# Optimization experiments

Measured on AMD Instinct MI355X. Metric: run time of the kernel, lower is better.

Reference implementation:

```python
import jax, jax.numpy as jnp
import numpy as np

LN_EPS = 1e-5

def _layernorm(w, g, b):
    mu = jnp.mean(w, axis=-1, keepdims=True)
    var = jnp.mean(jnp.square(w - mu), axis=-1, keepdims=True)
    return (w - mu) * jax.lax.rsqrt(var + LN_EPS) * g + b

def _ligru_layer(x, W, U, g, b):
    # x: [B, T, F]; W: [2H, F]; U: [2H, H]
    B = x.shape[0]
    H = U.shape[1]
    w = jnp.einsum('btf,hf->bth', x, W)          # [B, T, 2H]
    w = _layernorm(w, g, b)
    h0 = jnp.zeros((B, H), dtype=x.dtype)

    def step(h, w_t):                            # w_t: [B, 2H]
        gates = w_t + h @ U.T
        at, zt = gates[:, :H], gates[:, H:]
        zt = jax.nn.sigmoid(zt)
        hcand = jax.nn.relu(at)
        h = zt * h + (1.0 - zt) * hcand
        return h, h

    _, hs = jax.lax.scan(step, h0, jnp.swapaxes(w, 0, 1))  # hs: [T, B, H]
    return jnp.swapaxes(hs, 0, 1)                # [B, T, H]

def setup_inputs() -> dict:
    key = jax.random.key(0)
    ks = jax.random.split(key, 5)
    B, T, F, H = 16, 1500, 80, 512
    x = jax.random.normal(ks[0], (B, T, F), dtype=jnp.float32)
    W0 = jax.random.normal(ks[1], (2 * H, F), dtype=jnp.float32) / np.sqrt(F)
    U0 = jax.random.normal(ks[2], (2 * H, H), dtype=jnp.float32) / np.sqrt(H)
    W1 = jax.random.normal(ks[3], (2 * H, H), dtype=jnp.float32) / np.sqrt(H)
    U1 = jax.random.normal(ks[4], (2 * H, H), dtype=jnp.float32) / np.sqrt(H)
    g0 = jnp.ones((2 * H,), jnp.float32); b0 = jnp.zeros((2 * H,), jnp.float32)
    g1 = jnp.ones((2 * H,), jnp.float32); b1 = jnp.zeros((2 * H,), jnp.float32)
    return {"x": x, "W0": W0, "U0": U0, "g0": g0, "b0": b0,
            "W1": W1, "U1": U1, "g1": g1, "b1": b1}

def reference(x, W0, U0, g0, b0, W1, U1, g1, b1):
    h = _ligru_layer(x, W0, U0, g0, b0)
    h = _ligru_layer(h, W1, U1, g1, b1)
    return h
```

## Files before the change

kernel.cpp:

```cpp
#include <hip/hip_runtime.h>
#include <cstddef>
#include <cstdint>

#define kB 16
#define kT 1500
#define kF 80
#define kH 512
#define kGG 1024
#define kM (kB * kT)

__global__ __launch_bounds__(256) void gemm_nt_k(
    const float* __restrict__ A, const float* __restrict__ Bt,
    float* __restrict__ C, int K) {
  __shared__ float As[16][68];
  __shared__ float Bs[16][68];
  const int tid = threadIdx.x;
  const int m0 = blockIdx.x * 64;
  const int n0 = blockIdx.y * 64;
  const int tx = tid & 15;
  const int ty = tid >> 4;
  const int r  = tid >> 2;
  const int q  = tid & 3;
  float acc[4][4] = {};
  for (int k0 = 0; k0 < K; k0 += 16) {
    const float4 va = *(const float4*)&A [(size_t)(m0 + r) * K + k0 + q * 4];
    const float4 vb = *(const float4*)&Bt[(size_t)(n0 + r) * K + k0 + q * 4];
    __syncthreads();
    As[q * 4 + 0][r] = va.x; As[q * 4 + 1][r] = va.y;
    As[q * 4 + 2][r] = va.z; As[q * 4 + 3][r] = va.w;
    Bs[q * 4 + 0][r] = vb.x; Bs[q * 4 + 1][r] = vb.y;
    Bs[q * 4 + 2][r] = vb.z; Bs[q * 4 + 3][r] = vb.w;
    __syncthreads();
#pragma unroll
    for (int kk = 0; kk < 16; ++kk) {
      const float4 a = *(const float4*)&As[kk][ty * 4];
      const float4 b = *(const float4*)&Bs[kk][tx * 4];
      acc[0][0] += a.x * b.x; acc[0][1] += a.x * b.y; acc[0][2] += a.x * b.z; acc[0][3] += a.x * b.w;
      acc[1][0] += a.y * b.x; acc[1][1] += a.y * b.y; acc[1][2] += a.y * b.z; acc[1][3] += a.y * b.w;
      acc[2][0] += a.z * b.x; acc[2][1] += a.z * b.y; acc[2][2] += a.z * b.z; acc[2][3] += a.z * b.w;
      acc[3][0] += a.w * b.x; acc[3][1] += a.w * b.y; acc[3][2] += a.w * b.z; acc[3][3] += a.w * b.w;
    }
  }
#pragma unroll
  for (int i = 0; i < 4; ++i) {
    float4 o;
    o.x = acc[i][0]; o.y = acc[i][1]; o.z = acc[i][2]; o.w = acc[i][3];
    *(float4*)&C[(size_t)(m0 + ty * 4 + i) * kGG + n0 + tx * 4] = o;
  }
}

__global__ __launch_bounds__(256) void ln_rows(
    float* __restrict__ w, const float* __restrict__ g,
    const float* __restrict__ bb) {
  const int row = blockIdx.x;
  float4* p = (float4*)(w + (size_t)row * kGG);
  const int tid = threadIdx.x;
  float4 v = p[tid];
  float s  = v.x + v.y + v.z + v.w;
  float s2 = v.x * v.x + v.y * v.y + v.z * v.z + v.w * v.w;
#pragma unroll
  for (int off = 32; off >= 1; off >>= 1) {
    s  += __shfl_down(s, off);
    s2 += __shfl_down(s2, off);
  }
  __shared__ float red[8];
  const int lane = tid & 63, wv = tid >> 6;
  if (lane == 0) { red[wv] = s; red[4 + wv] = s2; }
  __syncthreads();
  s  = red[0] + red[1] + red[2] + red[3];
  s2 = red[4] + red[5] + red[6] + red[7];
  const float mu  = s * (1.f / kGG);
  const float var = s2 * (1.f / kGG) - mu * mu;
  const float rs  = rsqrtf(var + 1e-5f);
  const float4 gg = ((const float4*)g)[tid];
  const float4 bv = ((const float4*)bb)[tid];
  v.x = (v.x - mu) * rs * gg.x + bv.x;
  v.y = (v.y - mu) * rs * gg.y + bv.y;
  v.z = (v.z - mu) * rs * gg.z + bv.z;
  v.w = (v.w - mu) * rs * gg.w + bv.w;
  p[tid] = v;
}

__global__ __launch_bounds__(256, 1) void ligru_scan(
    const float* __restrict__ wn,
    const float* __restrict__ U,
    float* __restrict__ hist) {
  const int blk  = blockIdx.x;
  const int b    = blk >> 4;
  const int jblk = blk & 15;
  const int tid  = threadIdx.x;
  const int ks   = tid & 7;
  const int jj   = tid >> 3;
  const int j    = jblk * 32 + jj;
  const int k0   = ks * 64;

  __shared__ float hsh[2][8 * 68];

  float4 ua[16], uz[16];
#pragma unroll
  for (int q = 0; q < 16; ++q) {
    ua[q] = *(const float4*)&U[(size_t)j * kH + k0 + q * 4];
    uz[q] = *(const float4*)&U[(size_t)(j + kH) * kH + k0 + q * 4];
  }

  const float* wrow = wn + (size_t)b * kT * kGG;
  float* hrow = hist + (size_t)b * kT * kH;

  const int w0 = 2 * tid;
  const int lc = (w0 >> 6) * 68 + (w0 & 63);

  float hprev = 0.f;

  for (int t = 0; t < kT; ++t) {
    float wa = 0.f, wz = 0.f;
    if (ks == 0) {
      wa = wrow[(size_t)t * kGG + j];
      wz = wrow[(size_t)t * kGG + kH + j];
    }

    float* dst = hsh[t & 1];
    if (t == 0) {
      *(float2*)&dst[lc] = make_float2(0.f, 0.f);
    } else {
      const int* hp = (const int*)(hrow + (size_t)(t - 1) * kH);
      int v0, v1;
      do {
        v0 = __hip_atomic_load(hp + w0,     __ATOMIC_RELAXED,
                               __HIP_MEMORY_SCOPE_AGENT);
        v1 = __hip_atomic_load(hp + w0 + 1, __ATOMIC_RELAXED,
                               __HIP_MEMORY_SCOPE_AGENT);
      } while ((v0 | v1) < 0);
      *(float2*)&dst[lc] = make_float2(__int_as_float(v0), __int_as_float(v1));
    }
    __syncthreads();

    const float* src = dst + ks * 68;
    float ga = 0.f, gz = 0.f;
#pragma unroll
    for (int q = 0; q < 16; ++q) {
      const float4 h4 = *(const float4*)&src[q * 4];
      ga += h4.x * ua[q].x + h4.y * ua[q].y + h4.z * ua[q].z + h4.w * ua[q].w;
      gz += h4.x * uz[q].x + h4.y * uz[q].y + h4.z * uz[q].z + h4.w * uz[q].w;
    }
#pragma unroll
    for (int off = 1; off < 8; off <<= 1) {
      ga += __shfl_xor(ga, off);
      gz += __shfl_xor(gz, off);
    }

    if (ks == 0) {
      const float a    = wa + ga;
      const float z    = wz + gz;
      const float zt   = 1.f / (1.f + __expf(-z));
      const float hc   = fmaxf(a, 0.f);
      const float hnew = zt * hprev + (1.f - zt) * hc;
      hprev = hnew;
      __hip_atomic_store((int*)&hrow[(size_t)t * kH + j], __float_as_int(hnew),
                         __ATOMIC_RELAXED, __HIP_MEMORY_SCOPE_AGENT);
    }
  }
}

extern "C" void kernel_launch(void* const* d_in, const int* in_sizes, int n_in,
                              void* d_out, int out_size, void* d_ws,
                              size_t ws_size, hipStream_t stream) {
  const float* x  = (const float*)d_in[0];
  const float* W0 = (const float*)d_in[1];
  const float* U0 = (const float*)d_in[2];
  const float* g0 = (const float*)d_in[3];
  const float* b0 = (const float*)d_in[4];
  const float* W1 = (const float*)d_in[5];
  const float* U1 = (const float*)d_in[6];
  const float* g1 = (const float*)d_in[7];
  const float* b1 = (const float*)d_in[8];
  float* out = (float*)d_out;

  float* w = (float*)d_ws;

  const size_t out_bytes = (size_t)kM * kH * sizeof(float);

  hipMemsetAsync(out, 0xFF, out_bytes, stream);
  gemm_nt_k<<<dim3(kM / 64, kGG / 64), 256, 0, stream>>>(x, W0, w, kF);
  ln_rows<<<kM, 256, 0, stream>>>(w, g0, b0);
  {
    const float* wn_p = w;
    const float* U_p  = U0;
    float* h_p = out;
    void* args[] = {&wn_p, &U_p, &h_p};
    hipLaunchCooperativeKernel((const void*)ligru_scan, dim3(256), dim3(256),
                               args, 0, stream);
  }

  gemm_nt_k<<<dim3(kM / 64, kGG / 64), 256, 0, stream>>>(out, W1, w, kH);
  ln_rows<<<kM, 256, 0, stream>>>(w, g1, b1);
  hipMemsetAsync(out, 0xFF, out_bytes, stream);
  {
    const float* wn_p = w;
    const float* U_p  = U1;
    float* h_p = out;
    void* args[] = {&wn_p, &U_p, &h_p};
    hipLaunchCooperativeKernel((const void*)ligru_scan, dim3(256), dim3(256),
                               args, 0, stream);
  }
}
```

Before: 5.896 ms.

## Use inline-asm cache-scoped polling loads and interleave batch across blocks

Replaces the two relaxed atomic loads in the spin-wait with a single 64-bit global load carrying explicit cache-coherence bits (sc0, alternating with sc0 sc1 while spinning), so polling for the previous timestep's hidden state is cheaper and observes remote writes. The block-to-(batch, column-block) mapping is swapped so that blocks sharing a batch row are spread across the grid, which changes where the producers and consumers of each batch sit. Empty asm barriers pin the U weights in registers. Correctness depends on the sc0-only load eventually seeing other CUs' stores, which relies on undocumented cache behaviour.

```diff
diff --git a/kernel.cpp b/kernel.cpp
--- a/kernel.cpp
+++ b/kernel.cpp
@@ -8,6 +8,21 @@
 #define kH 512
 #define kGG 1024
 #define kM (kB * kT)
+
+typedef int v2i __attribute__((ext_vector_type(2)));
+
+__device__ __forceinline__ v2i poll_ld(const int* p, bool deep) {
+  v2i v;
+  if (deep)
+    asm volatile("global_load_dwordx2 %0, %1, off sc0 sc1\n\t"
+                 "s_waitcnt vmcnt(0)"
+                 : "=v"(v) : "v"(p) : "memory");
+  else
+    asm volatile("global_load_dwordx2 %0, %1, off sc0\n\t"
+                 "s_waitcnt vmcnt(0)"
+                 : "=v"(v) : "v"(p) : "memory");
+  return v;
+}
 
 __global__ __launch_bounds__(256) void gemm_nt_k(
     const float* __restrict__ A, const float* __restrict__ Bt,
@@ -86,8 +101,8 @@
     const float* __restrict__ U,
     float* __restrict__ hist) {
   const int blk  = blockIdx.x;
-  const int b    = blk >> 4;
-  const int jblk = blk & 15;
+  const int b    = blk & 15;
+  const int jblk = blk >> 4;
   const int tid  = threadIdx.x;
   const int ks   = tid & 7;
   const int jj   = tid >> 3;
@@ -101,6 +116,8 @@
   for (int q = 0; q < 16; ++q) {
     ua[q] = *(const float4*)&U[(size_t)j * kH + k0 + q * 4];
     uz[q] = *(const float4*)&U[(size_t)(j + kH) * kH + k0 + q * 4];
+    asm volatile("" : "+v"(ua[q].x), "+v"(ua[q].y), "+v"(ua[q].z), "+v"(ua[q].w));
+    asm volatile("" : "+v"(uz[q].x), "+v"(uz[q].y), "+v"(uz[q].z), "+v"(uz[q].w));
   }
 
   const float* wrow = wn + (size_t)b * kT * kGG;
@@ -122,15 +139,14 @@
     if (t == 0) {
       *(float2*)&dst[lc] = make_float2(0.f, 0.f);
     } else {
-      const int* hp = (const int*)(hrow + (size_t)(t - 1) * kH);
-      int v0, v1;
-      do {
-        v0 = __hip_atomic_load(hp + w0,     __ATOMIC_RELAXED,
-                               __HIP_MEMORY_SCOPE_AGENT);
-        v1 = __hip_atomic_load(hp + w0 + 1, __ATOMIC_RELAXED,
-                               __HIP_MEMORY_SCOPE_AGENT);
-      } while ((v0 | v1) < 0);
-      *(float2*)&dst[lc] = make_float2(__int_as_float(v0), __int_as_float(v1));
+      const int* hp = (const int*)(hrow + (size_t)(t - 1) * kH) + w0;
+      v2i v = poll_ld(hp, false);
+      int spins = 0;
+      while ((v.x | v.y) < 0) {
+        ++spins;
+        v = poll_ld(hp, (spins & 1) != 0);
+      }
+      *(float2*)&dst[lc] = make_float2(__int_as_float(v.x), __int_as_float(v.y));
     }
     __syncthreads();
 
```

Result: faster. 5.033 ms (-14.6%).
